# Performance work log

Measured on AMD Instinct MI355X. Metric: run time of the kernel, lower is better.

Reference implementation:

```python
import jax, jax.numpy as jnp
import numpy as np

N_LAYERS = 3


def setup_inputs() -> dict:
    key = jax.random.key(0)
    k1, k2, k3, k4 = jax.random.split(key, 4)
    user_emb = jax.random.normal(k1, (29858, 64), dtype=jnp.float32)
    item_emb = jax.random.normal(k2, (40981, 64), dtype=jnp.float32)
    v = jax.random.normal(k3, (70839, 512), dtype=jnp.float32)
    filters = jax.random.normal(k4, (N_LAYERS, 512), dtype=jnp.float32)
    return {"user_emb": user_emb, "item_emb": item_emb, "v": v, "filters": filters}


def reference(user_emb, item_emb, v, filters):
    # ego: [N, D], v: [N, F], filters: [L, F]
    n_users = user_emb.shape[0]
    ego = jnp.concatenate([user_emb, item_emb], axis=0)
    acc = ego  # running sum for the mean over (layers + 1) embeddings
    for k in range(filters.shape[0]):
        # V @ diag(f) @ V^T @ ego  ==  V @ (f[:, None] * (V^T @ ego))
        proj = v.T @ ego                      # [F, D]
        ego = v @ (filters[k][:, None] * proj)  # [N, D]
        acc = acc + ego
    all_emb = acc / (filters.shape[0] + 1)
    return all_emb[:n_users], all_emb[n_users:]
```

## Files before the change

kernel.cpp:

```cpp
#include <hip/hip_runtime.h>
#include <hip/hip_bf16.h>


#define N_USERS 29858
#define N_TOTAL 70839
#define DQ 64
#define FD 512
#define NPAD 71168

typedef __attribute__((ext_vector_type(8))) short short8;
typedef __attribute__((ext_vector_type(4))) float f32x4;
typedef unsigned int u32;
typedef unsigned short u16;

static __device__ __forceinline__ u32 f32u(float x){union{float f;u32 u;}a;a.f=x;return a.u;}
static __device__ __forceinline__ float uf32(u32 u){union{u32 u;float f;}a;a.u=u;return a.f;}
static __device__ __forceinline__ u32 pack_h(u32 x0, u32 x1){
  return __builtin_amdgcn_perm(x1, x0, 0x07060302u);
}
static __device__ __forceinline__ void split_pair(u32 x0, u32 x1, u32& hp, u32& lp) {
  hp = pack_h(x0, x1);
  u32 l0 = f32u(uf32(x0) - uf32(x0 & 0xFFFF0000u));
  u32 l1 = f32u(uf32(x1) - uf32(x1 & 0xFFFF0000u));
  lp = pack_h(l0, l1);
}
union U8x { u32 u[4]; short8 s; };

static __device__ __forceinline__ u16 bf16_rne(float x) {
  u32 u = f32u(x);
  return (u16)((u + 0x7FFFu + ((u >> 16) & 1u)) >> 16);
}
static __device__ __forceinline__ void split2(float x, u16& h, u16& l) {
  h = bf16_rne(x);
  l = bf16_rne(x - uf32(((u32)h) << 16));
}

static __device__ __forceinline__ void load_lds16(const float* g, float* l) {
  __builtin_amdgcn_global_load_lds(
      (const __attribute__((address_space(1))) u32*)(g),
      (__attribute__((address_space(3))) u32*)(l), 16, 0, 0);
}


__global__ __launch_bounds__(256) void init_kernel(
    const float* __restrict__ u, const float* __restrict__ it,
    float* __restrict__ out, u16* __restrict__ egoTb) {
  __shared__ float tile[64][65];
  const int n0 = blockIdx.x * 64;
  const int t = threadIdx.x;
  const int r = t >> 2, cbase = (t & 3) * 16;
  {
    int n = n0 + r;
    if (n < N_TOTAL) {
      const float* src = (n < N_USERS) ? (u + (size_t)n * DQ)
                                       : (it + (size_t)(n - N_USERS) * DQ);
#pragma unroll
      for (int q = 0; q < 4; ++q) {
        f32x4 val = *(const f32x4*)(src + cbase + q * 4);
        *(f32x4*)(out + (size_t)n * DQ + cbase + q * 4) = val;
        tile[r][cbase + q * 4 + 0] = val[0];
        tile[r][cbase + q * 4 + 1] = val[1];
        tile[r][cbase + q * 4 + 2] = val[2];
        tile[r][cbase + q * 4 + 3] = val[3];
      }
    } else {
#pragma unroll
      for (int q = 0; q < 4; ++q)
#pragma unroll
        for (int e = 0; e < 4; ++e) tile[r][cbase + q * 4 + e] = 0.f;
    }
  }
  __syncthreads();
  const int d = (t & 15) | ((t >> 6) << 4);
  const int nb = (t >> 4) & 3;
#pragma unroll
  for (int sl = 0; sl < 2; ++sl) {
    U8x H, L;
#pragma unroll
    for (int j = 0; j < 4; ++j) {
      u16 h0, l0, h1, l1;
      split2(tile[sl * 32 + nb * 8 + 2 * j][d], h0, l0);
      split2(tile[sl * 32 + nb * 8 + 2 * j + 1][d], h1, l1);
      H.u[j] = (u32)h0 | ((u32)h1 << 16);
      L.u[j] = (u32)l0 | ((u32)l1 << 16);
    }
    size_t base = (size_t)(blockIdx.x * 2 + sl) * 4096;
    *(short8*)(egoTb + base + (size_t)t * 8) = H.s;
    *(short8*)(egoTb + base + 2048 + (size_t)t * 8) = L.s;
  }
}

__global__ __launch_bounds__(256) void presplit_kernel(
    const float* __restrict__ v, u16* __restrict__ vbh, u16* __restrict__ vbl) {
  __shared__ float tile[64][65];
  const int n0 = blockIdx.x * 64;
  const int t = threadIdx.x;
  const int r = t >> 2, cbase = (t & 3) * 16;
  const int d = (t & 15) | ((t >> 6) << 4);
  const int nb = (t >> 4) & 3;
  for (int fo = 0; fo < FD; fo += 64) {
    __syncthreads();
    {
      int n = n0 + r;
      if (n < N_TOTAL) {
        const float* src = v + (size_t)n * FD + fo;
#pragma unroll
        for (int q = 0; q < 4; ++q) {
          f32x4 val = *(const f32x4*)(src + cbase + q * 4);
          tile[r][cbase + q * 4 + 0] = val[0];
          tile[r][cbase + q * 4 + 1] = val[1];
          tile[r][cbase + q * 4 + 2] = val[2];
          tile[r][cbase + q * 4 + 3] = val[3];
        }
      } else {
#pragma unroll
        for (int q = 0; q < 4; ++q)
#pragma unroll
          for (int e = 0; e < 4; ++e) tile[r][cbase + q * 4 + e] = 0.f;
      }
    }
    __syncthreads();
#pragma unroll
    for (int sl = 0; sl < 2; ++sl) {
      U8x H, L;
#pragma unroll
      for (int j = 0; j < 4; ++j) {
        u32 x0 = f32u(tile[sl * 32 + nb * 8 + 2 * j][d]);
        u32 x1 = f32u(tile[sl * 32 + nb * 8 + 2 * j + 1][d]);
        split_pair(x0, x1, H.u[j], L.u[j]);
      }
      size_t T = (size_t)((n0 >> 5) + sl) * 8 + (fo >> 6);
      *(short8*)(vbh + T * 2048 + (size_t)t * 8) = H.s;
      *(short8*)(vbl + T * 2048 + (size_t)t * 8) = L.s;
    }
  }
}

__global__ __launch_bounds__(256, 2) void gram_fast_kernel(
    const u16* __restrict__ vbh, const u16* __restrict__ vbl,
    const u16* __restrict__ egoTb, float* __restrict__ parts, int chunk) {
  __shared__ short8 HAh[1024];
  __shared__ short8 HAl[1024];
  __shared__ short8 HBh[256];
  __shared__ short8 HBl[256];

  const int job = blockIdx.x;
  const int n0c = blockIdx.y * chunk;
  const int nend = min(n0c + chunk, NPAD);
  const bool isC0 = (job >= 12);
  const int itile = isC0 ? (job - 12) : (job < 8 ? 0 : 1);
  const int fA = itile * 256;
  const int jcol = isC0 ? 0 : (job < 8 ? job : job - 4);
  const int colbase = jcol * 64;
  const bool reuseB = !isC0 && (colbase >= fA) && (colbase + 64 <= fA + 256);
  const bool stageB = !isC0 && !reuseB;
  const int cb0q = reuseB ? ((colbase - fA) >> 6) : 0;

  const int t = threadIdx.x;
  const int lane = t & 63, wv = t >> 6;
  const int m16 = lane & 15, quad = lane >> 4;
  const int ftA = fA >> 6;

  f32x4 acc[4][4];
#pragma unroll
  for (int a = 0; a < 4; ++a)
#pragma unroll
    for (int b = 0; b < 4; ++b) acc[a][b] = (f32x4){0.f, 0.f, 0.f, 0.f};

  short8 xAh[4], xAl[4], xBh, xBl;

  auto issue = [&](int n0) {
    size_t Tb = (size_t)(n0 >> 5) * 8;
    if (isC0) {
      xBh = *(const short8*)(egoTb + (size_t)(n0 >> 5) * 4096 + (size_t)t * 8);
      xBl = *(const short8*)(egoTb + (size_t)(n0 >> 5) * 4096 + 2048 + (size_t)t * 8);
    } else if (stageB) {
      size_t base = (Tb + (colbase >> 6)) * 2048 + (size_t)t * 8;
      xBh = *(const short8*)(vbh + base);
      xBl = *(const short8*)(vbl + base);
    }
#pragma unroll
    for (int seg = 0; seg < 4; ++seg) {
      size_t base = (Tb + ftA + seg) * 2048 + (size_t)t * 8;
      xAh[seg] = *(const short8*)(vbh + base);
      xAl[seg] = *(const short8*)(vbl + base);
    }
  };

  issue(n0c);

  for (int n0 = n0c; n0 < nend; n0 += 32) {
    asm volatile("s_barrier" ::: "memory");

#pragma unroll
    for (int seg = 0; seg < 4; ++seg) {
      HAh[seg * 256 + t] = xAh[seg];
      HAl[seg * 256 + t] = xAl[seg];
    }
    if (stageB || isC0) {
      HBh[t] = xBh;
      HBl[t] = xBl;
    }

    if (n0 + 32 < nend) issue(n0 + 32);

    asm volatile("s_waitcnt lgkmcnt(0)" ::: "memory");
    asm volatile("s_barrier" ::: "memory");

    short8 ah[4], al[4];
#pragma unroll
    for (int mt = 0; mt < 4; ++mt) {
      int u = m16 + mt * 64 + wv * 256 + quad * 16;
      ah[mt] = HAh[u];
      al[mt] = HAl[u];
    }
#pragma unroll
    for (int ct = 0; ct < 4; ++ct) {
      short8 bh, bl;
      if (reuseB) {
        int u = m16 + ct * 64 + cb0q * 256 + quad * 16;
        bh = HAh[u]; bl = HAl[u];
      } else {
        int u = m16 + ct * 64 + quad * 16;
        bh = HBh[u]; bl = HBl[u];
      }
#pragma unroll
      for (int mt = 0; mt < 4; ++mt) {
        acc[mt][ct] = __builtin_amdgcn_mfma_f32_16x16x32_bf16(ah[mt], bh, acc[mt][ct], 0, 0, 0);
        acc[mt][ct] = __builtin_amdgcn_mfma_f32_16x16x32_bf16(ah[mt], bl, acc[mt][ct], 0, 0, 0);
        acc[mt][ct] = __builtin_amdgcn_mfma_f32_16x16x32_bf16(al[mt], bh, acc[mt][ct], 0, 0, 0);
      }
    }
  }

  float* pb = parts + (size_t)blockIdx.y * (512 * 576);
  const int cb = isC0 ? 512 : colbase;
#pragma unroll
  for (int mt = 0; mt < 4; ++mt) {
    int row = fA + wv * 64 + mt * 16 + quad * 4;
#pragma unroll
    for (int ct = 0; ct < 4; ++ct) {
      int col = cb + ct * 16 + m16;
#pragma unroll
      for (int reg = 0; reg < 4; ++reg)
        pb[(size_t)(row + reg) * 576 + col] = acc[mt][ct][reg];
    }
  }
}

__global__ __launch_bounds__(256, 2) void gram_split_kernel(
    const float* __restrict__ v, const u16* __restrict__ egoTb,
    float* __restrict__ parts, int chunk) {
  __shared__ short8 HAh[1024];
  __shared__ short8 HAl[1024];
  __shared__ short8 HBh[256];
  __shared__ short8 HBl[256];

  const int job = blockIdx.x;
  const int n0c = blockIdx.y * chunk;
  const int nend = min(n0c + chunk, NPAD);
  const bool isC0 = (job >= 12);
  const int itile = isC0 ? (job - 12) : (job < 8 ? 0 : 1);
  const int fA = itile * 256;
  const int jcol = isC0 ? 0 : (job < 8 ? job : job - 4);
  const int colbase = jcol * 64;
  const bool reuseB = !isC0 && (colbase >= fA) && (colbase + 64 <= fA + 256);
  const bool stageB = !isC0 && !reuseB;
  const int cb0q = reuseB ? ((colbase - fA) >> 6) : 0;

  const int t = threadIdx.x;
  const int lane = t & 63, wv = t >> 6;
  const int m16 = lane & 15, quad = lane >> 4;
  const int fl = lane, nq = wv;

  f32x4 acc[4][4];
#pragma unroll
  for (int a = 0; a < 4; ++a)
#pragma unroll
    for (int b = 0; b < 4; ++b) acc[a][b] = (f32x4){0.f, 0.f, 0.f, 0.f};

  u32 xA[4][8];
  u32 xB[8];
  short8 xBh, xBl;

  auto issue = [&](int n0) {
    if (isC0) {
      xBh = *(const short8*)(egoTb + (size_t)(n0 >> 5) * 4096 + (size_t)t * 8);
      xBl = *(const short8*)(egoTb + (size_t)(n0 >> 5) * 4096 + 2048 + (size_t)t * 8);
    }
#pragma unroll
    for (int seg = 0; seg < 4; ++seg)
#pragma unroll
      for (int r = 0; r < 8; ++r) {
        int n = n0 + nq * 8 + r;
        xA[seg][r] = (n < N_TOTAL) ? f32u(v[(size_t)n * FD + fA + seg * 64 + fl]) : 0u;
      }
    if (stageB) {
#pragma unroll
      for (int r = 0; r < 8; ++r) {
        int n = n0 + nq * 8 + r;
        xB[r] = (n < N_TOTAL) ? f32u(v[(size_t)n * FD + colbase + fl]) : 0u;
      }
    }
  };

  issue(n0c);

  for (int n0 = n0c; n0 < nend; n0 += 32) {
    asm volatile("s_barrier" ::: "memory");

    const int uw = (fl & 15) + ((fl >> 4) & 3) * 64 + nq * 16;
#pragma unroll
    for (int seg = 0; seg < 4; ++seg) {
      U8x H, L;
#pragma unroll
      for (int p = 0; p < 4; ++p)
        split_pair(xA[seg][2 * p], xA[seg][2 * p + 1], H.u[p], L.u[p]);
      HAh[uw + seg * 256] = H.s;
      HAl[uw + seg * 256] = L.s;
    }
    if (stageB) {
      U8x H, L;
#pragma unroll
      for (int p = 0; p < 4; ++p)
        split_pair(xB[2 * p], xB[2 * p + 1], H.u[p], L.u[p]);
      HBh[uw] = H.s;
      HBl[uw] = L.s;
    } else if (isC0) {
      HBh[t] = xBh;
      HBl[t] = xBl;
    }

    if (n0 + 32 < nend) issue(n0 + 32);

    asm volatile("s_waitcnt lgkmcnt(0)" ::: "memory");
    asm volatile("s_barrier" ::: "memory");

    short8 ah[4], al[4];
#pragma unroll
    for (int mt = 0; mt < 4; ++mt) {
      int u = m16 + mt * 64 + wv * 256 + quad * 16;
      ah[mt] = HAh[u];
      al[mt] = HAl[u];
    }
#pragma unroll
    for (int ct = 0; ct < 4; ++ct) {
      short8 bh, bl;
      if (reuseB) {
        int u = m16 + ct * 64 + cb0q * 256 + quad * 16;
        bh = HAh[u]; bl = HAl[u];
      } else {
        int u = m16 + ct * 64 + quad * 16;
        bh = HBh[u]; bl = HBl[u];
      }
#pragma unroll
      for (int mt = 0; mt < 4; ++mt) {
        acc[mt][ct] = __builtin_amdgcn_mfma_f32_16x16x32_bf16(ah[mt], bh, acc[mt][ct], 0, 0, 0);
        acc[mt][ct] = __builtin_amdgcn_mfma_f32_16x16x32_bf16(ah[mt], bl, acc[mt][ct], 0, 0, 0);
        acc[mt][ct] = __builtin_amdgcn_mfma_f32_16x16x32_bf16(al[mt], bh, acc[mt][ct], 0, 0, 0);
      }
    }
  }

  float* pb = parts + (size_t)blockIdx.y * (512 * 576);
  const int cb = isC0 ? 512 : colbase;
#pragma unroll
  for (int mt = 0; mt < 4; ++mt) {
    int row = fA + wv * 64 + mt * 16 + quad * 4;
#pragma unroll
    for (int ct = 0; ct < 4; ++ct) {
      int col = cb + ct * 16 + m16;
#pragma unroll
      for (int reg = 0; reg < 4; ++reg)
        pb[(size_t)(row + reg) * 576 + col] = acc[mt][ct][reg];
    }
  }
}

__global__ __launch_bounds__(256) void finalize_kernel(
    const float* __restrict__ parts, int nc,
    float* __restrict__ G, float* __restrict__ c0) {
  int idx = blockIdx.x * 256 + threadIdx.x;
  int r = idx / 576, c = idx % 576;
  float s = 0.f;
  if (c >= 512) {
    for (int p = 0; p < nc; ++p) s += parts[(size_t)p * (512 * 576) + r * 576 + c];
    c0[r * 64 + (c - 512)] = s;
  } else {
    bool direct = (c >> 6) >= 4 * (r >> 8);
    int rr = direct ? r : c, cc = direct ? c : r;
    for (int p = 0; p < nc; ++p) s += parts[(size_t)p * (512 * 576) + rr * 576 + cc];
    G[r * 512 + c] = s;
  }
}

__global__ __launch_bounds__(256) void apply_g_kernel(
    const float* __restrict__ G, const float* __restrict__ filt,
    const float* __restrict__ cin, float* __restrict__ cout) {
  __shared__ float red[4][64];
  const int t = threadIdx.x;
  const int i = blockIdx.x;
  const int sub = t >> 6, d = t & 63;
  float s = 0.f;
#pragma unroll 8
  for (int j = sub * 128; j < (sub + 1) * 128; ++j)
    s += G[i * 512 + j] * (filt[j] * cin[j * 64 + d]);
  red[sub][d] = s;
  __syncthreads();
  if (sub == 0)
    cout[i * 64 + d] = red[0][d] + red[1][d] + red[2][d] + red[3][d];
}

__global__ __launch_bounds__(256) void prep_wt_kernel(
    const float* __restrict__ filters, const float* __restrict__ c0,
    const float* __restrict__ c1, const float* __restrict__ c2,
    u16* __restrict__ wt_h) {
  int idx = blockIdx.x * 256 + threadIdx.x;
  int d = idx >> 9, f = idx & 511;
  float w = filters[f] * c0[f * 64 + d] + filters[512 + f] * c1[f * 64 + d] +
            filters[1024 + f] * c2[f * 64 + d];
  wt_h[d * FD + f] = bf16_rne(w);
}

__global__ __launch_bounds__(256) void expand_kernel(
    const float* __restrict__ v, const u16* __restrict__ wt_h,
    float* __restrict__ out) {
  __shared__ float raw[2][128 * 64];
  const int t = threadIdx.x;
  const int lane = t & 63, wv = t >> 6;
  const int m16 = lane & 15, quad = lane >> 4;
  const int nb = blockIdx.x * 128;

  f32x4 acc[2][4];
#pragma unroll
  for (int a = 0; a < 2; ++a)
#pragma unroll
    for (int b = 0; b < 4; ++b) acc[a][b] = (f32x4){0.f, 0.f, 0.f, 0.f};

  auto stage = [&](int buf, int fs) {
#pragma unroll
    for (int g = 0; g < 8; ++g) {
      int rl = g * 4 + (lane >> 4);
      int sw = rl & 7;
      int grow = min(nb + wv * 32 + rl, N_TOTAL - 1);
      const float* gp = v + (size_t)grow * FD + fs + (((lane & 15) ^ sw) << 2);
      load_lds16(gp, &raw[buf][(wv * 32 + g * 4) * 64]);
    }
  };

  stage(0, 0);
  for (int it8 = 0; it8 < 8; ++it8) {
    const int buf = it8 & 1, fs = it8 * 64;
    short8 pbh[2][4];
#pragma unroll
    for (int k = 0; k < 2; ++k)
#pragma unroll
      for (int ct = 0; ct < 4; ++ct) {
        const size_t off = (size_t)(ct * 16 + m16) * FD + fs + k * 32 + quad * 8;
        pbh[k][ct] = *(const short8*)(wt_h + off);
      }
    asm volatile("" ::: "memory");
    if (it8 + 1 < 8) {
      stage(buf ^ 1, fs + 64);
      asm volatile("s_waitcnt vmcnt(16)" ::: "memory");
    } else {
      asm volatile("s_waitcnt vmcnt(8)" ::: "memory");
    }
#pragma unroll
    for (int k0i = 0; k0i < 2; ++k0i) {
      short8 ah[2];
#pragma unroll
      for (int mt = 0; mt < 2; ++mt) {
        const float* rb = &raw[buf][(wv * 32 + mt * 16 + m16) * 64];
        const int sw = m16 & 7;
        const int j0 = k0i * 8 + quad * 2;
        f32x4 xa = *(const f32x4*)(rb + ((j0 ^ sw) << 2));
        f32x4 xb = *(const f32x4*)(rb + (((j0 + 1) ^ sw) << 2));
        U8x H;
        H.u[0] = pack_h(f32u(xa[0]), f32u(xa[1]));
        H.u[1] = pack_h(f32u(xa[2]), f32u(xa[3]));
        H.u[2] = pack_h(f32u(xb[0]), f32u(xb[1]));
        H.u[3] = pack_h(f32u(xb[2]), f32u(xb[3]));
        ah[mt] = H.s;
      }
#pragma unroll
      for (int ct = 0; ct < 4; ++ct)
#pragma unroll
        for (int mt = 0; mt < 2; ++mt)
          acc[mt][ct] = __builtin_amdgcn_mfma_f32_16x16x32_bf16(ah[mt], pbh[k0i][ct], acc[mt][ct], 0, 0, 0);
    }
  }

#pragma unroll
  for (int mt = 0; mt < 2; ++mt) {
    int nrow = nb + wv * 32 + mt * 16 + quad * 4;
#pragma unroll
    for (int ct = 0; ct < 4; ++ct) {
      int d = ct * 16 + m16;
#pragma unroll
      for (int reg = 0; reg < 4; ++reg) {
        int n = nrow + reg;
        if (n < N_TOTAL) {
          float* op = out + (size_t)n * DQ + d;
          *op = (*op + acc[mt][ct][reg]) * 0.25f;
        }
      }
    }
  }
}

extern "C" void kernel_launch(void* const* d_in, const int* in_sizes, int n_in,
                              void* d_out, int out_size, void* d_ws, size_t ws_size,
                              hipStream_t stream) {
  const float* user_emb = (const float*)d_in[0];
  const float* item_emb = (const float*)d_in[1];
  const float* v        = (const float*)d_in[2];
  const float* filters  = (const float*)d_in[3];
  float* out = (float*)d_out;

  const size_t EGOTB_BYTES = (size_t)(NPAD / 32) * 8192;
  const size_t VB_BYTES    = (size_t)NPAD * FD * 2;
  const size_t SMALL_BYTES = (512 * 512 + 3 * 512 * 64) * 4 + DQ * FD * 2;
  const size_t PART_BYTES  = (size_t)512 * 576 * 4;

  size_t fixed_fast = EGOTB_BYTES + 2 * VB_BYTES + SMALL_BYTES;
  int nc_fast = ws_size > fixed_fast ? (int)((ws_size - fixed_fast) / PART_BYTES) : 0;
  const bool fast = (nc_fast >= 28);

  int nc;
  if (fast) {
    nc = nc_fast > 35 ? 35 : nc_fast;
  } else {
    size_t fixed = EGOTB_BYTES + SMALL_BYTES;
    size_t avail = ws_size > fixed ? ws_size - fixed : 0;
    nc = (int)(avail / PART_BYTES);
    if (nc > 35) nc = 35;
    if (nc < 1) nc = 1;
  }
  int chunk = ((NPAD + nc - 1) / nc + 31) & ~31;
  int ncA = (NPAD + chunk - 1) / chunk;

  char* p = (char*)d_ws;
  u16* egoTb = (u16*)p;            p += EGOTB_BYTES;
  u16* vbh = nullptr; u16* vbl = nullptr;
  if (fast) { vbh = (u16*)p; p += VB_BYTES; vbl = (u16*)p; p += VB_BYTES; }
  float* parts = (float*)p;        p += (size_t)ncA * PART_BYTES;
  float* G     = (float*)p;        p += (size_t)512 * 512 * 4;
  float* c0    = (float*)p;        p += (size_t)512 * 64 * 4;
  float* c1    = (float*)p;        p += (size_t)512 * 64 * 4;
  float* c2    = (float*)p;        p += (size_t)512 * 64 * 4;
  u16* wt_h    = (u16*)p;

  init_kernel<<<NPAD / 64, 256, 0, stream>>>(user_emb, item_emb, out, egoTb);
  if (fast) {
    presplit_kernel<<<NPAD / 64, 256, 0, stream>>>(v, vbh, vbl);
    gram_fast_kernel<<<dim3(14, ncA), 256, 0, stream>>>(vbh, vbl, egoTb, parts, chunk);
  } else {
    gram_split_kernel<<<dim3(14, ncA), 256, 0, stream>>>(v, egoTb, parts, chunk);
  }
  finalize_kernel<<<(512 * 576) / 256, 256, 0, stream>>>(parts, ncA, G, c0);
  apply_g_kernel<<<512, 256, 0, stream>>>(G, filters, c0, c1);
  apply_g_kernel<<<512, 256, 0, stream>>>(G, filters + 512, c1, c2);
  prep_wt_kernel<<<128, 256, 0, stream>>>(filters, c0, c1, c2, wt_h);
  expand_kernel<<<NPAD / 128, 256, 0, stream>>>(v, wt_h, out);
}
```

Measured before the change: 511.1 us.

## Drop bf16 hi/lo split in Gram kernel, use single bf16 MFMA pass

The fast Gram path now keeps only a round-to-nearest bf16 copy of V instead of hi/lo split pairs, so each tile needs one MFMA instead of three and half the staging traffic and LDS. Presplit is rewritten to read V columns directly without an LDS transpose, occupancy is raised to 3 blocks per SM, and the chunk cap is raised. The exchange is a large precision loss in V^T V and V^T ego, which may exceed tolerance.

```diff
diff --git a/kernel.cpp b/kernel.cpp
--- a/kernel.cpp
+++ b/kernel.cpp
@@ -91,58 +91,47 @@
 }
 
 __global__ __launch_bounds__(256) void presplit_kernel(
-    const float* __restrict__ v, u16* __restrict__ vbh, u16* __restrict__ vbl) {
-  __shared__ float tile[64][65];
-  const int n0 = blockIdx.x * 64;
+    const float* __restrict__ v, u16* __restrict__ vbh) {
+  const int n0 = blockIdx.x * 32;
   const int t = threadIdx.x;
-  const int r = t >> 2, cbase = (t & 3) * 16;
-  const int d = (t & 15) | ((t >> 6) << 4);
+  const int fp = (t & 15) | ((t >> 6) << 4);
   const int nb = (t >> 4) & 3;
-  for (int fo = 0; fo < FD; fo += 64) {
-    __syncthreads();
-    {
-      int n = n0 + r;
-      if (n < N_TOTAL) {
-        const float* src = v + (size_t)n * FD + fo;
-#pragma unroll
-        for (int q = 0; q < 4; ++q) {
-          f32x4 val = *(const f32x4*)(src + cbase + q * 4);
-          tile[r][cbase + q * 4 + 0] = val[0];
-          tile[r][cbase + q * 4 + 1] = val[1];
-          tile[r][cbase + q * 4 + 2] = val[2];
-          tile[r][cbase + q * 4 + 3] = val[3];
-        }
-      } else {
-#pragma unroll
-        for (int q = 0; q < 4; ++q)
-#pragma unroll
-          for (int e = 0; e < 4; ++e) tile[r][cbase + q * 4 + e] = 0.f;
-      }
-    }
-    __syncthreads();
-#pragma unroll
-    for (int sl = 0; sl < 2; ++sl) {
-      U8x H, L;
+  const int nbase = n0 + nb * 8;
+  const size_t Tb = (size_t)(n0 >> 5) * 8;
+  if (nbase + 8 <= N_TOTAL) {
+#pragma unroll
+    for (int tf = 0; tf < 8; ++tf) {
+      const float* col = v + (size_t)nbase * FD + tf * 64 + fp;
+      U8x H;
 #pragma unroll
       for (int j = 0; j < 4; ++j) {
-        u32 x0 = f32u(tile[sl * 32 + nb * 8 + 2 * j][d]);
-        u32 x1 = f32u(tile[sl * 32 + nb * 8 + 2 * j + 1][d]);
-        split_pair(x0, x1, H.u[j], L.u[j]);
-      }
-      size_t T = (size_t)((n0 >> 5) + sl) * 8 + (fo >> 6);
-      *(short8*)(vbh + T * 2048 + (size_t)t * 8) = H.s;
-      *(short8*)(vbl + T * 2048 + (size_t)t * 8) = L.s;
-    }
-  }
-}
-
-__global__ __launch_bounds__(256, 2) void gram_fast_kernel(
-    const u16* __restrict__ vbh, const u16* __restrict__ vbl,
-    const u16* __restrict__ egoTb, float* __restrict__ parts, int chunk) {
+        u16 h0 = bf16_rne(col[(size_t)(2 * j) * FD]);
+        u16 h1 = bf16_rne(col[(size_t)(2 * j + 1) * FD]);
+        H.u[j] = (u32)h0 | ((u32)h1 << 16);
+      }
+      *(short8*)(vbh + (Tb + tf) * 2048 + (size_t)t * 8) = H.s;
+    }
+  } else {
+#pragma unroll
+    for (int tf = 0; tf < 8; ++tf) {
+      U8x H;
+#pragma unroll
+      for (int j = 0; j < 4; ++j) {
+        int na = nbase + 2 * j, nbv = nbase + 2 * j + 1;
+        float xa = (na < N_TOTAL) ? v[(size_t)na * FD + tf * 64 + fp] : 0.f;
+        float xb = (nbv < N_TOTAL) ? v[(size_t)nbv * FD + tf * 64 + fp] : 0.f;
+        H.u[j] = (u32)bf16_rne(xa) | ((u32)bf16_rne(xb) << 16);
+      }
+      *(short8*)(vbh + (Tb + tf) * 2048 + (size_t)t * 8) = H.s;
+    }
+  }
+}
+
+__global__ __launch_bounds__(256, 3) void gram_fast_kernel(
+    const u16* __restrict__ vbh, const u16* __restrict__ egoTb,
+    float* __restrict__ parts, int chunk) {
   __shared__ short8 HAh[1024];
-  __shared__ short8 HAl[1024];
   __shared__ short8 HBh[256];
-  __shared__ short8 HBl[256];
 
   const int job = blockIdx.x;
   const int n0c = blockIdx.y * chunk;
@@ -167,24 +156,18 @@
 #pragma unroll
     for (int b = 0; b < 4; ++b) acc[a][b] = (f32x4){0.f, 0.f, 0.f, 0.f};
 
-  short8 xAh[4], xAl[4], xBh, xBl;
+  short8 xAh[4], xBh;
 
   auto issue = [&](int n0) {
     size_t Tb = (size_t)(n0 >> 5) * 8;
     if (isC0) {
       xBh = *(const short8*)(egoTb + (size_t)(n0 >> 5) * 4096 + (size_t)t * 8);
-      xBl = *(const short8*)(egoTb + (size_t)(n0 >> 5) * 4096 + 2048 + (size_t)t * 8);
     } else if (stageB) {
-      size_t base = (Tb + (colbase >> 6)) * 2048 + (size_t)t * 8;
-      xBh = *(const short8*)(vbh + base);
-      xBl = *(const short8*)(vbl + base);
-    }
-#pragma unroll
-    for (int seg = 0; seg < 4; ++seg) {
-      size_t base = (Tb + ftA + seg) * 2048 + (size_t)t * 8;
-      xAh[seg] = *(const short8*)(vbh + base);
-      xAl[seg] = *(const short8*)(vbl + base);
-    }
+      xBh = *(const short8*)(vbh + (Tb + (colbase >> 6)) * 2048 + (size_t)t * 8);
+    }
+#pragma unroll
+    for (int seg = 0; seg < 4; ++seg)
+      xAh[seg] = *(const short8*)(vbh + (Tb + ftA + seg) * 2048 + (size_t)t * 8);
   };
 
   issue(n0c);
@@ -193,43 +176,31 @@
     asm volatile("s_barrier" ::: "memory");
 
 #pragma unroll
-    for (int seg = 0; seg < 4; ++seg) {
+    for (int seg = 0; seg < 4; ++seg)
       HAh[seg * 256 + t] = xAh[seg];
-      HAl[seg * 256 + t] = xAl[seg];
-    }
-    if (stageB || isC0) {
+    if (stageB || isC0)
       HBh[t] = xBh;
-      HBl[t] = xBl;
-    }
 
     if (n0 + 32 < nend) issue(n0 + 32);
 
     asm volatile("s_waitcnt lgkmcnt(0)" ::: "memory");
     asm volatile("s_barrier" ::: "memory");
 
-    short8 ah[4], al[4];
-#pragma unroll
-    for (int mt = 0; mt < 4; ++mt) {
-      int u = m16 + mt * 64 + wv * 256 + quad * 16;
-      ah[mt] = HAh[u];
-      al[mt] = HAl[u];
-    }
+    short8 ah[4];
+#pragma unroll
+    for (int mt = 0; mt < 4; ++mt)
+      ah[mt] = HAh[m16 + mt * 64 + wv * 256 + quad * 16];
 #pragma unroll
     for (int ct = 0; ct < 4; ++ct) {
-      short8 bh, bl;
+      short8 bh;
       if (reuseB) {
-        int u = m16 + ct * 64 + cb0q * 256 + quad * 16;
-        bh = HAh[u]; bl = HAl[u];
+        bh = HAh[m16 + ct * 64 + cb0q * 256 + quad * 16];
       } else {
-        int u = m16 + ct * 64 + quad * 16;
-        bh = HBh[u]; bl = HBl[u];
-      }
-#pragma unroll
-      for (int mt = 0; mt < 4; ++mt) {
+        bh = HBh[m16 + ct * 64 + quad * 16];
+      }
+#pragma unroll
+      for (int mt = 0; mt < 4; ++mt)
         acc[mt][ct] = __builtin_amdgcn_mfma_f32_16x16x32_bf16(ah[mt], bh, acc[mt][ct], 0, 0, 0);
-        acc[mt][ct] = __builtin_amdgcn_mfma_f32_16x16x32_bf16(ah[mt], bl, acc[mt][ct], 0, 0, 0);
-        acc[mt][ct] = __builtin_amdgcn_mfma_f32_16x16x32_bf16(al[mt], bh, acc[mt][ct], 0, 0, 0);
-      }
     }
   }
 
@@ -523,13 +494,13 @@
   const size_t SMALL_BYTES = (512 * 512 + 3 * 512 * 64) * 4 + DQ * FD * 2;
   const size_t PART_BYTES  = (size_t)512 * 576 * 4;
 
-  size_t fixed_fast = EGOTB_BYTES + 2 * VB_BYTES + SMALL_BYTES;
+  size_t fixed_fast = EGOTB_BYTES + VB_BYTES + SMALL_BYTES;
   int nc_fast = ws_size > fixed_fast ? (int)((ws_size - fixed_fast) / PART_BYTES) : 0;
   const bool fast = (nc_fast >= 28);
 
   int nc;
   if (fast) {
-    nc = nc_fast > 35 ? 35 : nc_fast;
+    nc = nc_fast > 56 ? 56 : nc_fast;
   } else {
     size_t fixed = EGOTB_BYTES + SMALL_BYTES;
     size_t avail = ws_size > fixed ? ws_size - fixed : 0;
@@ -542,8 +513,8 @@
 
   char* p = (char*)d_ws;
   u16* egoTb = (u16*)p;            p += EGOTB_BYTES;
-  u16* vbh = nullptr; u16* vbl = nullptr;
-  if (fast) { vbh = (u16*)p; p += VB_BYTES; vbl = (u16*)p; p += VB_BYTES; }
+  u16* vbh = nullptr;
+  if (fast) { vbh = (u16*)p; p += VB_BYTES; }
   float* parts = (float*)p;        p += (size_t)ncA * PART_BYTES;
   float* G     = (float*)p;        p += (size_t)512 * 512 * 4;
   float* c0    = (float*)p;        p += (size_t)512 * 64 * 4;
@@ -553,8 +524,8 @@
 
   init_kernel<<<NPAD / 64, 256, 0, stream>>>(user_emb, item_emb, out, egoTb);
   if (fast) {
-    presplit_kernel<<<NPAD / 64, 256, 0, stream>>>(v, vbh, vbl);
-    gram_fast_kernel<<<dim3(14, ncA), 256, 0, stream>>>(vbh, vbl, egoTb, parts, chunk);
+    presplit_kernel<<<NPAD / 32, 256, 0, stream>>>(v, vbh);
+    gram_fast_kernel<<<dim3(14, ncA), 256, 0, stream>>>(vbh, egoTb, parts, chunk);
   } else {
     gram_split_kernel<<<dim3(14, ncA), 256, 0, stream>>>(v, egoTb, parts, chunk);
   }
```

New measurement: 445.6 us. 1.15x faster.
